# Performance work log

Measured on AMD Instinct MI355X. Metric: run time of the kernel, lower is better.

The kernel has to match this reference:

```python
import jax, jax.numpy as jnp
import numpy as np
from jax import lax

DIM = 128  # per-head dim used for scaling


def setup_inputs() -> dict:
    key = jax.random.key(0)
    ks = jax.random.split(key, 6)
    B, S, D = 16, 2048, DIM
    query = jax.random.normal(ks[0], (B, S, D), dtype=jnp.float32)
    k = jax.random.normal(ks[1], (B, S, D), dtype=jnp.float32)
    value = jax.random.normal(ks[2], (B, S, D), dtype=jnp.float32)
    mask = jax.random.randint(ks[3], (B, 1, S), 0, 2, dtype=jnp.int32)
    conv_w = jax.random.normal(ks[4], (B, 1, 3, 3), dtype=jnp.float32) * 0.1  # depthwise 3x3, OIHW
    conv_b = jax.random.normal(ks[5], (B,), dtype=jnp.float32) * 0.1
    return {"query": query, "key": k, "value": value, "mask": mask,
            "conv_w": conv_w, "conv_b": conv_b}


def reference(query, key, value, mask, conv_w, conv_b):
    B = query.shape[0]
    # score: (B, Sq, Sk)
    score = jnp.einsum('bqd,bkd->bqk', query, key) / jnp.float32(np.sqrt(DIM))
    # depthwise 3x3 conv over the score map; score treated as (C=B, H=Sq, W=Sk)
    conv = lax.conv_general_dilated(
        score[None],                      # (1, B, Sq, Sk)
        conv_w,                           # (B, 1, 3, 3)
        window_strides=(1, 1), padding='SAME',
        feature_group_count=B,
        dimension_numbers=('NCHW', 'OIHW', 'NCHW'))[0]
    conv = jax.nn.relu(conv + conv_b[:, None, None])
    conv_score = score + conv
    conv_score = jnp.where(mask == 0, jnp.float32(-1e9), conv_score)
    atten = jax.nn.softmax(conv_score, axis=-1)  # attn_drop=0.0 -> identity
    context = jnp.einsum('bqk,bkd->bqd', atten, value)
    return (context, atten)
```

## Files before the change

### kernel.cpp

```cpp
#include <hip/hip_runtime.h>
#include <stdint.h>

#define B_BATCH 16
#define SEQ     2048
#define DIMD    128
#define QT_OUT  14
#define SROWS   16
#define TILES_PB 147
#define SCALE   0.08838834764831845f
#define L2E     1.4426950408889634f

#define SC_STRIDE 4096
#define LDS_TOTAL (SROWS * SC_STRIDE)

typedef __attribute__((ext_vector_type(8))) short bf16x8;
typedef __attribute__((ext_vector_type(4))) float f32x4;

__device__ __forceinline__ unsigned short f2bf(float f) {
  union { float f; uint32_t u; } v; v.f = f;
  uint32_t u = v.u;
  return (unsigned short)((u + 0x7FFFu + ((u >> 16) & 1u)) >> 16);
}
__device__ __forceinline__ float bf2f(unsigned short h) {
  union { uint32_t u; float f; } v; v.u = ((uint32_t)h) << 16;
  return v.f;
}

__global__ __launch_bounds__(256) void cvt_bf16(const float* __restrict__ in,
                                                unsigned short* __restrict__ out) {
  const size_t i = (size_t)blockIdx.x * 256 + threadIdx.x;
  const float4 a = *(const float4*)(in + i * 8);
  const float4 b = *(const float4*)(in + i * 8 + 4);
  uint4 o;
  o.x = (uint32_t)f2bf(a.x) | ((uint32_t)f2bf(a.y) << 16);
  o.y = (uint32_t)f2bf(a.z) | ((uint32_t)f2bf(a.w) << 16);
  o.z = (uint32_t)f2bf(b.x) | ((uint32_t)f2bf(b.y) << 16);
  o.w = (uint32_t)f2bf(b.z) | ((uint32_t)f2bf(b.w) << 16);
  *(uint4*)(out + i * 8) = o;
}

__global__ __launch_bounds__(256) void transpose_v(const float* __restrict__ V,
                                                   unsigned short* __restrict__ Vt) {
  __shared__ float tl[64][65];
  const int b  = blockIdx.x >> 6;
  const int kt = (blockIdx.x & 63) >> 1;
  const int dt = blockIdx.x & 1;
  const int k0 = kt * 64, d0 = dt * 64;
  const int tid = threadIdx.x;
  const int r = tid >> 4, c4 = (tid & 15) * 4;
  const float* Vb = V + (size_t)b * SEQ * DIMD;
#pragma unroll
  for (int ii = 0; ii < 4; ++ii) {
    const int row = ii * 16 + r;
    float4 v = *(const float4*)(Vb + (size_t)(k0 + row) * DIMD + d0 + c4);
    tl[row][c4 + 0] = v.x; tl[row][c4 + 1] = v.y;
    tl[row][c4 + 2] = v.z; tl[row][c4 + 3] = v.w;
  }
  __syncthreads();
  unsigned short* VtB = Vt + (size_t)b * DIMD * SEQ;
#pragma unroll
  for (int ii = 0; ii < 4; ++ii) {
    const int drow = ii * 16 + r;
    ushort4 o;
    o.x = f2bf(tl[c4 + 0][drow]); o.y = f2bf(tl[c4 + 1][drow]);
    o.z = f2bf(tl[c4 + 2][drow]); o.w = f2bf(tl[c4 + 3][drow]);
    *(ushort4*)(VtB + (size_t)(d0 + drow) * SEQ + k0 + c4) = o;
  }
}

__global__ __launch_bounds__(512, 4) void fused_attn(
    const float* __restrict__ Q, const unsigned short* __restrict__ Kb,
    const unsigned short* __restrict__ Vt, const int* __restrict__ msk,
    const float* __restrict__ cw, const float* __restrict__ cbv,
    float* __restrict__ ctx, float* __restrict__ attn) {
  __shared__ __align__(16) char smem[LDS_TOTAL];

  const int bid = blockIdx.x;
  const int b  = bid / TILES_PB;
  const int t  = bid - b * TILES_PB;
  const int g0 = t * QT_OUT;
  const int tid = threadIdx.x;
  const int w = tid >> 6, lane = tid & 63, l15 = lane & 15, hi = lane >> 4;

  float w9[9];
#pragma unroll
  for (int i = 0; i < 9; ++i) w9[i] = cw[b * 9 + i];
  const float bias = cbv[b];

  uint32_t mb = 0;
  {
    const int* mp = msk + b * SEQ;
#pragma unroll
    for (int jb = 0; jb < 4; ++jb) {
      int4 a = *(const int4*)(mp + jb * 512 + lane * 8);
      int4 bq = *(const int4*)(mp + jb * 512 + lane * 8 + 4);
      mb |= (a.x  != 0 ? 1u : 0u) << (jb * 8 + 0);
      mb |= (a.y  != 0 ? 1u : 0u) << (jb * 8 + 1);
      mb |= (a.z  != 0 ? 1u : 0u) << (jb * 8 + 2);
      mb |= (a.w  != 0 ? 1u : 0u) << (jb * 8 + 3);
      mb |= (bq.x != 0 ? 1u : 0u) << (jb * 8 + 4);
      mb |= (bq.y != 0 ? 1u : 0u) << (jb * 8 + 5);
      mb |= (bq.z != 0 ? 1u : 0u) << (jb * 8 + 6);
      mb |= (bq.w != 0 ? 1u : 0u) << (jb * 8 + 7);
    }
  }

  bf16x8 aq[4];
  {
    int grow = g0 - 1 + l15;
    grow = grow < 0 ? 0 : (grow > SEQ - 1 ? SEQ - 1 : grow);
    const float* qp = Q + ((size_t)(b * SEQ + grow)) * DIMD + hi * 8;
#pragma unroll
    for (int ks = 0; ks < 4; ++ks) {
      float4 x = *(const float4*)(qp + ks * 32);
      float4 y = *(const float4*)(qp + ks * 32 + 4);
      bf16x8 f;
      f[0] = (short)f2bf(x.x); f[1] = (short)f2bf(x.y);
      f[2] = (short)f2bf(x.z); f[3] = (short)f2bf(x.w);
      f[4] = (short)f2bf(y.x); f[5] = (short)f2bf(y.y);
      f[6] = (short)f2bf(y.z); f[7] = (short)f2bf(y.w);
      aq[ks] = f;
    }
  }

  {
    const unsigned short* KbB = Kb + (size_t)b * SEQ * DIMD;
    const int k0w = w * 256;
#pragma unroll 2
    for (int kc = 0; kc < 16; ++kc) {
      const int k0 = k0w + kc * 16;
      const unsigned short* kp = KbB + (size_t)(k0 + l15) * DIMD + hi * 8;
      bf16x8 bk0 = *(const bf16x8*)(kp);
      bf16x8 bk1 = *(const bf16x8*)(kp + 32);
      bf16x8 bk2 = *(const bf16x8*)(kp + 64);
      bf16x8 bk3 = *(const bf16x8*)(kp + 96);
      f32x4 acc = {0.f, 0.f, 0.f, 0.f};
      acc = __builtin_amdgcn_mfma_f32_16x16x32_bf16(aq[0], bk0, acc, 0, 0, 0);
      acc = __builtin_amdgcn_mfma_f32_16x16x32_bf16(aq[1], bk1, acc, 0, 0, 0);
      acc = __builtin_amdgcn_mfma_f32_16x16x32_bf16(aq[2], bk2, acc, 0, 0, 0);
      acc = __builtin_amdgcn_mfma_f32_16x16x32_bf16(aq[3], bk3, acc, 0, 0, 0);
      const int colb = (k0 + l15) * 2;
#pragma unroll
      for (int r = 0; r < 4; ++r) {
        const int row = hi * 4 + r;
        *(unsigned short*)(smem + row * SC_STRIDE + (colb ^ ((row & 7) << 4))) =
            f2bf(acc[r] * SCALE);
      }
    }
  }
  __syncthreads();

  const int nrows = (SEQ - g0) < QT_OUT ? (SEQ - g0) : QT_OUT;
  float* attnB = attn + (size_t)b * SEQ * SEQ;

  for (int sp = 0; sp < 2; ++sp) {
    const int i = sp * 8 + w;
    const bool act = (i < nrows);
    float p[32];
    float inv = 0.f;
    if (act) {
      const int g = g0 + i;
      const bool vtop = (g > 0), vbot = (g + 1 < SEQ);
#pragma unroll
      for (int jb = 0; jb < 4; ++jb) {
        float m[3][8], Lv[3], Rv[3];
#pragma unroll
        for (int r = 0; r < 3; ++r) {
          const bool v = (r == 1) || ((r == 0) ? vtop : vbot);
          if (v) {
            const int row = i + r;
            const int rs = row * SC_STRIDE, sw = (row & 7) << 4;
            bf16x8 vv = *(const bf16x8*)(smem + rs + ((jb * 1024 + lane * 16) ^ sw));
#pragma unroll
            for (int c = 0; c < 8; ++c) m[r][c] = bf2f((unsigned short)vv[c]);
            float le = 0.f, re = 0.f;
            if (jb > 0)
              le = bf2f(*(const unsigned short*)(smem + rs + (((jb * 512 - 1) * 2) ^ sw)));
            if (jb < 3)
              re = bf2f(*(const unsigned short*)(smem + rs + (((jb * 512 + 512) * 2) ^ sw)));
            const float lsh = __shfl_up(m[r][7], 1);
            const float rsh = __shfl_down(m[r][0], 1);
            Lv[r] = (lane == 0)  ? le : lsh;
            Rv[r] = (lane == 63) ? re : rsh;
          } else {
#pragma unroll
            for (int c = 0; c < 8; ++c) m[r][c] = 0.f;
            Lv[r] = 0.f; Rv[r] = 0.f;
          }
        }
#pragma unroll
        for (int c = 0; c < 8; ++c) {
          float cv = 0.f;
#pragma unroll
          for (int r = 0; r < 3; ++r) {
            const float lft = (c == 0) ? Lv[r] : m[r][c - 1];
            const float rgt = (c == 7) ? Rv[r] : m[r][c + 1];
            cv += w9[r * 3 + 0] * lft + w9[r * 3 + 1] * m[r][c] + w9[r * 3 + 2] * rgt;
          }
          const float val = m[1][c] + fmaxf(cv + bias, 0.f);
          p[jb * 8 + c] = ((mb >> (jb * 8 + c)) & 1u) ? val : -1e9f;
        }
      }
      float mx = p[0];
#pragma unroll
      for (int k = 1; k < 32; ++k) mx = fmaxf(mx, p[k]);
#pragma unroll
      for (int o = 1; o < 64; o <<= 1) mx = fmaxf(mx, __shfl_xor(mx, o, 64));
      float Z = 0.f;
#pragma unroll
      for (int k = 0; k < 32; ++k) {
        p[k] = __builtin_amdgcn_exp2f((p[k] - mx) * L2E);
        Z += p[k];
      }
#pragma unroll
      for (int o = 1; o < 64; o <<= 1) Z += __shfl_xor(Z, o, 64);
      inv = 1.0f / Z;
      float* arow = attnB + (size_t)g * SEQ;
#pragma unroll
      for (int jb = 0; jb < 4; ++jb) {
        const int colb = jb * 512 + lane * 8;
        *(float4*)(arow + colb) = make_float4(p[jb * 8 + 0] * inv, p[jb * 8 + 1] * inv,
                                              p[jb * 8 + 2] * inv, p[jb * 8 + 3] * inv);
        *(float4*)(arow + colb + 4) = make_float4(p[jb * 8 + 4] * inv, p[jb * 8 + 5] * inv,
                                                  p[jb * 8 + 6] * inv, p[jb * 8 + 7] * inv);
      }
    }
    __syncthreads();
    if (act) {
      const int rs = i * SC_STRIDE, sw = (i & 7) << 4;
#pragma unroll
      for (int jb = 0; jb < 4; ++jb) {
        bf16x8 h;
#pragma unroll
        for (int c = 0; c < 8; ++c) h[c] = (short)f2bf(p[jb * 8 + c] * inv);
        *(bf16x8*)(smem + rs + ((jb * 1024 + lane * 16) ^ sw)) = h;
      }
    }
    __syncthreads();
  }

  {
    const unsigned short* vp =
        Vt + (size_t)b * DIMD * SEQ + (size_t)(16 * w + l15) * SEQ + hi * 8;
    const int arow = l15;
    const int abase = arow * SC_STRIDE;
    const int asw = (arow & 7) << 4;
    f32x4 acc0 = {0.f, 0.f, 0.f, 0.f}, acc1 = {0.f, 0.f, 0.f, 0.f};
#pragma unroll 2
    for (int kc = 0; kc < 32; ++kc) {
      const int k0 = kc * 64;
      bf16x8 a0 = *(const bf16x8*)(smem + abase + (((k0      ) * 2 + hi * 16) ^ asw));
      bf16x8 b0 = *(const bf16x8*)(vp + k0);
      acc0 = __builtin_amdgcn_mfma_f32_16x16x32_bf16(a0, b0, acc0, 0, 0, 0);
      bf16x8 a1 = *(const bf16x8*)(smem + abase + (((k0 + 32) * 2 + hi * 16) ^ asw));
      bf16x8 b1 = *(const bf16x8*)(vp + k0 + 32);
      acc1 = __builtin_amdgcn_mfma_f32_16x16x32_bf16(a1, b1, acc1, 0, 0, 0);
    }
    const int col = 16 * w + l15;
#pragma unroll
    for (int r = 0; r < 4; ++r) {
      const int row = hi * 4 + r;
      const int g = g0 + row;
      if (row < QT_OUT && g < SEQ)
        ctx[((size_t)(b * SEQ + g)) * DIMD + col] = acc0[r] + acc1[r];
    }
  }
}

extern "C" void kernel_launch(void* const* d_in, const int* in_sizes, int n_in,
                              void* d_out, int out_size, void* d_ws, size_t ws_size,
                              hipStream_t stream) {
  const float* Q  = (const float*)d_in[0];
  const float* K  = (const float*)d_in[1];
  const float* V  = (const float*)d_in[2];
  const int* msk  = (const int*)d_in[3];
  const float* cw = (const float*)d_in[4];
  const float* cb = (const float*)d_in[5];
  float* ctx  = (float*)d_out;
  float* attn = ctx + (size_t)B_BATCH * SEQ * DIMD;
  unsigned short* Kb = (unsigned short*)d_ws;
  unsigned short* Vt = Kb + (size_t)B_BATCH * SEQ * DIMD;

  cvt_bf16<<<2048, 256, 0, stream>>>(K, Kb);
  transpose_v<<<B_BATCH * 64, 256, 0, stream>>>(V, Vt);
  fused_attn<<<B_BATCH * TILES_PB, 512, 0, stream>>>(Q, Kb, Vt, msk, cw, cb, ctx, attn);
}
```

Baseline: 413.3 us.

## Defer attention-row stores to kernel end using nontemporal writes from LDS

New measurement: 366.9 us. 11.2% less time.

```diff
diff --git a/kernel.cpp b/kernel.cpp
--- a/kernel.cpp
+++ b/kernel.cpp
@@ -76,8 +76,8 @@
   __shared__ __align__(16) char smem[LDS_TOTAL];
 
   const int bid = blockIdx.x;
-  const int b  = bid / TILES_PB;
-  const int t  = bid - b * TILES_PB;
+  const int b  = bid & 15;
+  const int t  = bid >> 4;
   const int g0 = t * QT_OUT;
   const int tid = threadIdx.x;
   const int w = tid >> 6, lane = tid & 63, l15 = lane & 15, hi = lane >> 4;
@@ -126,7 +126,7 @@
   {
     const unsigned short* KbB = Kb + (size_t)b * SEQ * DIMD;
     const int k0w = w * 256;
-#pragma unroll 2
+#pragma unroll 4
     for (int kc = 0; kc < 16; ++kc) {
       const int k0 = k0w + kc * 16;
       const unsigned short* kp = KbB + (size_t)(k0 + l15) * DIMD + hi * 8;
@@ -151,7 +151,6 @@
   __syncthreads();
 
   const int nrows = (SEQ - g0) < QT_OUT ? (SEQ - g0) : QT_OUT;
-  float* attnB = attn + (size_t)b * SEQ * SEQ;
 
   for (int sp = 0; sp < 2; ++sp) {
     const int i = sp * 8 + w;
@@ -215,15 +214,6 @@
 #pragma unroll
       for (int o = 1; o < 64; o <<= 1) Z += __shfl_xor(Z, o, 64);
       inv = 1.0f / Z;
-      float* arow = attnB + (size_t)g * SEQ;
-#pragma unroll
-      for (int jb = 0; jb < 4; ++jb) {
-        const int colb = jb * 512 + lane * 8;
-        *(float4*)(arow + colb) = make_float4(p[jb * 8 + 0] * inv, p[jb * 8 + 1] * inv,
-                                              p[jb * 8 + 2] * inv, p[jb * 8 + 3] * inv);
-        *(float4*)(arow + colb + 4) = make_float4(p[jb * 8 + 4] * inv, p[jb * 8 + 5] * inv,
-                                                  p[jb * 8 + 6] * inv, p[jb * 8 + 7] * inv);
-      }
     }
     __syncthreads();
     if (act) {
@@ -242,11 +232,10 @@
   {
     const unsigned short* vp =
         Vt + (size_t)b * DIMD * SEQ + (size_t)(16 * w + l15) * SEQ + hi * 8;
-    const int arow = l15;
-    const int abase = arow * SC_STRIDE;
-    const int asw = (arow & 7) << 4;
+    const int abase = l15 * SC_STRIDE;
+    const int asw = (l15 & 7) << 4;
     f32x4 acc0 = {0.f, 0.f, 0.f, 0.f}, acc1 = {0.f, 0.f, 0.f, 0.f};
-#pragma unroll 2
+#pragma unroll 4
     for (int kc = 0; kc < 32; ++kc) {
       const int k0 = kc * 64;
       bf16x8 a0 = *(const bf16x8*)(smem + abase + (((k0      ) * 2 + hi * 16) ^ asw));
@@ -262,7 +251,31 @@
       const int row = hi * 4 + r;
       const int g = g0 + row;
       if (row < QT_OUT && g < SEQ)
-        ctx[((size_t)(b * SEQ + g)) * DIMD + col] = acc0[r] + acc1[r];
+        __builtin_nontemporal_store(acc0[r] + acc1[r],
+                                    &ctx[((size_t)(b * SEQ + g)) * DIMD + col]);
+    }
+  }
+
+  {
+    float* attnB = attn + (size_t)b * SEQ * SEQ;
+#pragma unroll
+    for (int sp = 0; sp < 2; ++sp) {
+      const int i = sp * 8 + w;
+      if (i < nrows) {
+        const int g = g0 + i;
+        float* arow = attnB + (size_t)g * SEQ;
+        const int rs = i * SC_STRIDE, sw = (i & 7) << 4;
+#pragma unroll
+        for (int jb = 0; jb < 8; ++jb) {
+          uint2 hv = *(const uint2*)(smem + rs + ((jb * 512 + lane * 8) ^ sw));
+          f32x4 o;
+          o[0] = bf2f((unsigned short)(hv.x & 0xffffu));
+          o[1] = bf2f((unsigned short)(hv.x >> 16));
+          o[2] = bf2f((unsigned short)(hv.y & 0xffffu));
+          o[3] = bf2f((unsigned short)(hv.y >> 16));
+          __builtin_nontemporal_store(o, (f32x4*)(arow + jb * 256 + lane * 4));
+        }
+      }
     }
   }
 }
```

## Split fused attention into separate QK GEMM, conv-softmax, and PV GEMM kernels

Applied to the files above, without the earlier changes.

New measurement: 425.5 us. +3.0%, slower.

```diff
diff --git a/kernel.cpp b/kernel.cpp
--- a/kernel.cpp
+++ b/kernel.cpp
@@ -4,14 +4,8 @@
 #define B_BATCH 16
 #define SEQ     2048
 #define DIMD    128
-#define QT_OUT  14
-#define SROWS   16
-#define TILES_PB 147
 #define SCALE   0.08838834764831845f
 #define L2E     1.4426950408889634f
-
-#define SC_STRIDE 4096
-#define LDS_TOTAL (SROWS * SC_STRIDE)
 
 typedef __attribute__((ext_vector_type(8))) short bf16x8;
 typedef __attribute__((ext_vector_type(4))) float f32x4;
@@ -68,19 +62,68 @@
   }
 }
 
-__global__ __launch_bounds__(512, 4) void fused_attn(
-    const float* __restrict__ Q, const unsigned short* __restrict__ Kb,
-    const unsigned short* __restrict__ Vt, const int* __restrict__ msk,
+__global__ __launch_bounds__(512, 2) void qk_gemm(
+    const unsigned short* __restrict__ Qb, const unsigned short* __restrict__ Kb,
+    unsigned short* __restrict__ S) {
+  __shared__ __align__(16) char sm[128 * 256];
+  const int bid = blockIdx.x;
+  const int b = bid & 15, t = bid >> 4, tr = t & 15, tc = t >> 4;
+  const int tid = threadIdx.x;
+  const int w = tid >> 6, lane = tid & 63, l15 = lane & 15, hi = lane >> 4;
+  const int wr = w >> 2, wc = w & 3;
+
+  const unsigned short* Qp =
+      Qb + ((size_t)(b * SEQ) + tr * 128 + wr * 64) * DIMD;
+  const unsigned short* Kp =
+      Kb + ((size_t)(b * SEQ) + tc * 128 + wc * 32) * DIMD;
+
+  f32x4 acc[4][2] = {};
+#pragma unroll
+  for (int ks = 0; ks < 4; ++ks) {
+    bf16x8 aq[4], bk[2];
+#pragma unroll
+    for (int fr = 0; fr < 4; ++fr)
+      aq[fr] = *(const bf16x8*)(Qp + (size_t)(fr * 16 + l15) * DIMD + ks * 32 + hi * 8);
+#pragma unroll
+    for (int fc = 0; fc < 2; ++fc)
+      bk[fc] = *(const bf16x8*)(Kp + (size_t)(fc * 16 + l15) * DIMD + ks * 32 + hi * 8);
+#pragma unroll
+    for (int fr = 0; fr < 4; ++fr)
+#pragma unroll
+      for (int fc = 0; fc < 2; ++fc)
+        acc[fr][fc] = __builtin_amdgcn_mfma_f32_16x16x32_bf16(aq[fr], bk[fc], acc[fr][fc], 0, 0, 0);
+  }
+#pragma unroll
+  for (int fr = 0; fr < 4; ++fr)
+#pragma unroll
+    for (int fc = 0; fc < 2; ++fc)
+#pragma unroll
+      for (int r = 0; r < 4; ++r) {
+        const int row = wr * 64 + fr * 16 + hi * 4 + r;
+        const int colb = (wc * 32 + fc * 16 + l15) * 2;
+        *(unsigned short*)(sm + row * 256 + (colb ^ ((row & 7) << 4))) =
+            f2bf(acc[fr][fc][r] * SCALE);
+      }
+  __syncthreads();
+  unsigned short* Sp = S + ((size_t)(b * SEQ) + tr * 128) * SEQ + tc * 128;
+  const int rr = tid >> 4, cc = tid & 15;
+#pragma unroll
+  for (int p = 0; p < 4; ++p) {
+    const int row = p * 32 + rr;
+    bf16x8 v = *(const bf16x8*)(sm + row * 256 + ((cc * 16) ^ ((row & 7) << 4)));
+    *(bf16x8*)(Sp + (size_t)row * SEQ + cc * 8) = v;
+  }
+}
+
+__global__ __launch_bounds__(512, 1) void conv_softmax(
+    const unsigned short* __restrict__ S, const int* __restrict__ msk,
     const float* __restrict__ cw, const float* __restrict__ cbv,
-    float* __restrict__ ctx, float* __restrict__ attn) {
-  __shared__ __align__(16) char smem[LDS_TOTAL];
-
+    float* __restrict__ attn) {
   const int bid = blockIdx.x;
-  const int b  = bid / TILES_PB;
-  const int t  = bid - b * TILES_PB;
-  const int g0 = t * QT_OUT;
-  const int tid = threadIdx.x;
-  const int w = tid >> 6, lane = tid & 63, l15 = lane & 15, hi = lane >> 4;
+  const int b = bid & 15, rblk = bid >> 4;
+  const int tid = threadIdx.x;
+  const int w = tid >> 6, lane = tid & 63;
+  const int g = rblk * 8 + w;
 
   float w9[9];
 #pragma unroll
@@ -105,166 +148,112 @@
     }
   }
 
-  bf16x8 aq[4];
-  {
-    int grow = g0 - 1 + l15;
-    grow = grow < 0 ? 0 : (grow > SEQ - 1 ? SEQ - 1 : grow);
-    const float* qp = Q + ((size_t)(b * SEQ + grow)) * DIMD + hi * 8;
-#pragma unroll
-    for (int ks = 0; ks < 4; ++ks) {
-      float4 x = *(const float4*)(qp + ks * 32);
-      float4 y = *(const float4*)(qp + ks * 32 + 4);
-      bf16x8 f;
-      f[0] = (short)f2bf(x.x); f[1] = (short)f2bf(x.y);
-      f[2] = (short)f2bf(x.z); f[3] = (short)f2bf(x.w);
-      f[4] = (short)f2bf(y.x); f[5] = (short)f2bf(y.y);
-      f[6] = (short)f2bf(y.z); f[7] = (short)f2bf(y.w);
-      aq[ks] = f;
-    }
-  }
-
-  {
-    const unsigned short* KbB = Kb + (size_t)b * SEQ * DIMD;
-    const int k0w = w * 256;
-#pragma unroll 2
-    for (int kc = 0; kc < 16; ++kc) {
-      const int k0 = k0w + kc * 16;
-      const unsigned short* kp = KbB + (size_t)(k0 + l15) * DIMD + hi * 8;
-      bf16x8 bk0 = *(const bf16x8*)(kp);
-      bf16x8 bk1 = *(const bf16x8*)(kp + 32);
-      bf16x8 bk2 = *(const bf16x8*)(kp + 64);
-      bf16x8 bk3 = *(const bf16x8*)(kp + 96);
-      f32x4 acc = {0.f, 0.f, 0.f, 0.f};
-      acc = __builtin_amdgcn_mfma_f32_16x16x32_bf16(aq[0], bk0, acc, 0, 0, 0);
-      acc = __builtin_amdgcn_mfma_f32_16x16x32_bf16(aq[1], bk1, acc, 0, 0, 0);
-      acc = __builtin_amdgcn_mfma_f32_16x16x32_bf16(aq[2], bk2, acc, 0, 0, 0);
-      acc = __builtin_amdgcn_mfma_f32_16x16x32_bf16(aq[3], bk3, acc, 0, 0, 0);
-      const int colb = (k0 + l15) * 2;
-#pragma unroll
-      for (int r = 0; r < 4; ++r) {
-        const int row = hi * 4 + r;
-        *(unsigned short*)(smem + row * SC_STRIDE + (colb ^ ((row & 7) << 4))) =
-            f2bf(acc[r] * SCALE);
+  const unsigned short* Sb = S + (size_t)b * SEQ * SEQ;
+  const bool vtop = (g > 0), vbot = (g + 1 < SEQ);
+  float p[32];
+#pragma unroll
+  for (int jb = 0; jb < 4; ++jb) {
+    float m[3][8], Lv[3], Rv[3];
+#pragma unroll
+    for (int r = 0; r < 3; ++r) {
+      const bool v = (r == 1) || ((r == 0) ? vtop : vbot);
+      if (v) {
+        const unsigned short* srow = Sb + (size_t)(g - 1 + r) * SEQ;
+        bf16x8 vv = *(const bf16x8*)(srow + jb * 512 + lane * 8);
+#pragma unroll
+        for (int c = 0; c < 8; ++c) m[r][c] = bf2f((unsigned short)vv[c]);
+        float le = 0.f, re = 0.f;
+        if (jb > 0) le = bf2f(srow[jb * 512 - 1]);
+        if (jb < 3) re = bf2f(srow[jb * 512 + 512]);
+        const float lsh = __shfl_up(m[r][7], 1);
+        const float rsh = __shfl_down(m[r][0], 1);
+        Lv[r] = (lane == 0)  ? le : lsh;
+        Rv[r] = (lane == 63) ? re : rsh;
+      } else {
+#pragma unroll
+        for (int c = 0; c < 8; ++c) m[r][c] = 0.f;
+        Lv[r] = 0.f; Rv[r] = 0.f;
       }
     }
-  }
-  __syncthreads();
-
-  const int nrows = (SEQ - g0) < QT_OUT ? (SEQ - g0) : QT_OUT;
-  float* attnB = attn + (size_t)b * SEQ * SEQ;
-
-  for (int sp = 0; sp < 2; ++sp) {
-    const int i = sp * 8 + w;
-    const bool act = (i < nrows);
-    float p[32];
-    float inv = 0.f;
-    if (act) {
-      const int g = g0 + i;
-      const bool vtop = (g > 0), vbot = (g + 1 < SEQ);
-#pragma unroll
-      for (int jb = 0; jb < 4; ++jb) {
-        float m[3][8], Lv[3], Rv[3];
-#pragma unroll
-        for (int r = 0; r < 3; ++r) {
-          const bool v = (r == 1) || ((r == 0) ? vtop : vbot);
-          if (v) {
-            const int row = i + r;
-            const int rs = row * SC_STRIDE, sw = (row & 7) << 4;
-            bf16x8 vv = *(const bf16x8*)(smem + rs + ((jb * 1024 + lane * 16) ^ sw));
-#pragma unroll
-            for (int c = 0; c < 8; ++c) m[r][c] = bf2f((unsigned short)vv[c]);
-            float le = 0.f, re = 0.f;
-            if (jb > 0)
-              le = bf2f(*(const unsigned short*)(smem + rs + (((jb * 512 - 1) * 2) ^ sw)));
-            if (jb < 3)
-              re = bf2f(*(const unsigned short*)(smem + rs + (((jb * 512 + 512) * 2) ^ sw)));
-            const float lsh = __shfl_up(m[r][7], 1);
-            const float rsh = __shfl_down(m[r][0], 1);
-            Lv[r] = (lane == 0)  ? le : lsh;
-            Rv[r] = (lane == 63) ? re : rsh;
-          } else {
-#pragma unroll
-            for (int c = 0; c < 8; ++c) m[r][c] = 0.f;
-            Lv[r] = 0.f; Rv[r] = 0.f;
-          }
-        }
-#pragma unroll
-        for (int c = 0; c < 8; ++c) {
-          float cv = 0.f;
-#pragma unroll
-          for (int r = 0; r < 3; ++r) {
-            const float lft = (c == 0) ? Lv[r] : m[r][c - 1];
-            const float rgt = (c == 7) ? Rv[r] : m[r][c + 1];
-            cv += w9[r * 3 + 0] * lft + w9[r * 3 + 1] * m[r][c] + w9[r * 3 + 2] * rgt;
-          }
-          const float val = m[1][c] + fmaxf(cv + bias, 0.f);
-          p[jb * 8 + c] = ((mb >> (jb * 8 + c)) & 1u) ? val : -1e9f;
-        }
+#pragma unroll
+    for (int c = 0; c < 8; ++c) {
+      float cv = 0.f;
+#pragma unroll
+      for (int r = 0; r < 3; ++r) {
+        const float lft = (c == 0) ? Lv[r] : m[r][c - 1];
+        const float rgt = (c == 7) ? Rv[r] : m[r][c + 1];
+        cv += w9[r * 3 + 0] * lft + w9[r * 3 + 1] * m[r][c] + w9[r * 3 + 2] * rgt;
       }
-      float mx = p[0];
-#pragma unroll
-      for (int k = 1; k < 32; ++k) mx = fmaxf(mx, p[k]);
-#pragma unroll
-      for (int o = 1; o < 64; o <<= 1) mx = fmaxf(mx, __shfl_xor(mx, o, 64));
-      float Z = 0.f;
-#pragma unroll
-      for (int k = 0; k < 32; ++k) {
-        p[k] = __builtin_amdgcn_exp2f((p[k] - mx) * L2E);
-        Z += p[k];
-      }
-#pragma unroll
-      for (int o = 1; o < 64; o <<= 1) Z += __shfl_xor(Z, o, 64);
-      inv = 1.0f / Z;
-      float* arow = attnB + (size_t)g * SEQ;
-#pragma unroll
-      for (int jb = 0; jb < 4; ++jb) {
-        const int colb = jb * 512 + lane * 8;
-        *(float4*)(arow + colb) = make_float4(p[jb * 8 + 0] * inv, p[jb * 8 + 1] * inv,
-                                              p[jb * 8 + 2] * inv, p[jb * 8 + 3] * inv);
-        *(float4*)(arow + colb + 4) = make_float4(p[jb * 8 + 4] * inv, p[jb * 8 + 5] * inv,
-                                                  p[jb * 8 + 6] * inv, p[jb * 8 + 7] * inv);
-      }
-    }
-    __syncthreads();
-    if (act) {
-      const int rs = i * SC_STRIDE, sw = (i & 7) << 4;
-#pragma unroll
-      for (int jb = 0; jb < 4; ++jb) {
-        bf16x8 h;
-#pragma unroll
-        for (int c = 0; c < 8; ++c) h[c] = (short)f2bf(p[jb * 8 + c] * inv);
-        *(bf16x8*)(smem + rs + ((jb * 1024 + lane * 16) ^ sw)) = h;
-      }
-    }
-    __syncthreads();
-  }
-
-  {
-    const unsigned short* vp =
-        Vt + (size_t)b * DIMD * SEQ + (size_t)(16 * w + l15) * SEQ + hi * 8;
-    const int arow = l15;
-    const int abase = arow * SC_STRIDE;
-    const int asw = (arow & 7) << 4;
-    f32x4 acc0 = {0.f, 0.f, 0.f, 0.f}, acc1 = {0.f, 0.f, 0.f, 0.f};
-#pragma unroll 2
-    for (int kc = 0; kc < 32; ++kc) {
-      const int k0 = kc * 64;
-      bf16x8 a0 = *(const bf16x8*)(smem + abase + (((k0      ) * 2 + hi * 16) ^ asw));
-      bf16x8 b0 = *(const bf16x8*)(vp + k0);
-      acc0 = __builtin_amdgcn_mfma_f32_16x16x32_bf16(a0, b0, acc0, 0, 0, 0);
-      bf16x8 a1 = *(const bf16x8*)(smem + abase + (((k0 + 32) * 2 + hi * 16) ^ asw));
-      bf16x8 b1 = *(const bf16x8*)(vp + k0 + 32);
-      acc1 = __builtin_amdgcn_mfma_f32_16x16x32_bf16(a1, b1, acc1, 0, 0, 0);
-    }
-    const int col = 16 * w + l15;
+      const float val = m[1][c] + fmaxf(cv + bias, 0.f);
+      p[jb * 8 + c] = ((mb >> (jb * 8 + c)) & 1u) ? val : -1e9f;
+    }
+  }
+  float mx = p[0];
+#pragma unroll
+  for (int k = 1; k < 32; ++k) mx = fmaxf(mx, p[k]);
+#pragma unroll
+  for (int o = 1; o < 64; o <<= 1) mx = fmaxf(mx, __shfl_xor(mx, o, 64));
+  float Z = 0.f;
+#pragma unroll
+  for (int k = 0; k < 32; ++k) {
+    p[k] = __builtin_amdgcn_exp2f((p[k] - mx) * L2E);
+    Z += p[k];
+  }
+#pragma unroll
+  for (int o = 1; o < 64; o <<= 1) Z += __shfl_xor(Z, o, 64);
+  const float inv = 1.0f / Z;
+
+  float* arow = attn + (size_t)b * SEQ * SEQ + (size_t)g * SEQ;
+#pragma unroll
+  for (int jb = 0; jb < 4; ++jb) {
+    f32x4 o0, o1;
+    o0[0] = p[jb * 8 + 0] * inv; o0[1] = p[jb * 8 + 1] * inv;
+    o0[2] = p[jb * 8 + 2] * inv; o0[3] = p[jb * 8 + 3] * inv;
+    o1[0] = p[jb * 8 + 4] * inv; o1[1] = p[jb * 8 + 5] * inv;
+    o1[2] = p[jb * 8 + 6] * inv; o1[3] = p[jb * 8 + 7] * inv;
+    __builtin_nontemporal_store(o0, (f32x4*)(arow + jb * 512 + lane * 8));
+    __builtin_nontemporal_store(o1, (f32x4*)(arow + jb * 512 + lane * 8 + 4));
+  }
+}
+
+__global__ __launch_bounds__(512, 2) void pv_gemm(
+    const float* __restrict__ attn, const unsigned short* __restrict__ Vt,
+    float* __restrict__ ctx) {
+  const int bid = blockIdx.x;
+  const int b = bid & 15, rt = bid >> 4;
+  const int tid = threadIdx.x;
+  const int w = tid >> 6, lane = tid & 63, l15 = lane & 15, hi = lane >> 4;
+  const int wr = w >> 1, wc = w & 1;
+
+  const float* Ap =
+      attn + ((size_t)b * SEQ + rt * 64 + wr * 16 + l15) * SEQ + hi * 8;
+  const unsigned short* Vp = Vt + ((size_t)b * DIMD + wc * 64) * SEQ;
+
+  f32x4 acc[4] = {};
+#pragma unroll 4
+  for (int kk = 0; kk < 64; ++kk) {
+    const int k0 = kk * 32;
+    float4 x = *(const float4*)(Ap + k0);
+    float4 y = *(const float4*)(Ap + k0 + 4);
+    bf16x8 a;
+    a[0] = (short)f2bf(x.x); a[1] = (short)f2bf(x.y);
+    a[2] = (short)f2bf(x.z); a[3] = (short)f2bf(x.w);
+    a[4] = (short)f2bf(y.x); a[5] = (short)f2bf(y.y);
+    a[6] = (short)f2bf(y.z); a[7] = (short)f2bf(y.w);
+#pragma unroll
+    for (int fc = 0; fc < 4; ++fc) {
+      bf16x8 bv = *(const bf16x8*)(Vp + (size_t)(fc * 16 + l15) * SEQ + k0 + hi * 8);
+      acc[fc] = __builtin_amdgcn_mfma_f32_16x16x32_bf16(a, bv, acc[fc], 0, 0, 0);
+    }
+  }
+#pragma unroll
+  for (int fc = 0; fc < 4; ++fc)
 #pragma unroll
     for (int r = 0; r < 4; ++r) {
-      const int row = hi * 4 + r;
-      const int g = g0 + row;
-      if (row < QT_OUT && g < SEQ)
-        ctx[((size_t)(b * SEQ + g)) * DIMD + col] = acc0[r] + acc1[r];
-    }
-  }
+      const int row = rt * 64 + wr * 16 + hi * 4 + r;
+      const int col = wc * 64 + fc * 16 + l15;
+      ctx[((size_t)b * SEQ + row) * DIMD + col] = acc[fc][r];
+    }
 }
 
 extern "C" void kernel_launch(void* const* d_in, const int* in_sizes, int n_in,
@@ -278,10 +267,17 @@
   const float* cb = (const float*)d_in[5];
   float* ctx  = (float*)d_out;
   float* attn = ctx + (size_t)B_BATCH * SEQ * DIMD;
-  unsigned short* Kb = (unsigned short*)d_ws;
-  unsigned short* Vt = Kb + (size_t)B_BATCH * SEQ * DIMD;
-
+
+  const size_t nQK = (size_t)B_BATCH * SEQ * DIMD;
+  unsigned short* Qb = (unsigned short*)d_ws;
+  unsigned short* Kb = Qb + nQK;
+  unsigned short* Vt = Kb + nQK;
+  unsigned short* S  = Vt + nQK;
+
+  cvt_bf16<<<2048, 256, 0, stream>>>(Q, Qb);
   cvt_bf16<<<2048, 256, 0, stream>>>(K, Kb);
   transpose_v<<<B_BATCH * 64, 256, 0, stream>>>(V, Vt);
-  fused_attn<<<B_BATCH * TILES_PB, 512, 0, stream>>>(Q, Kb, Vt, msk, cw, cb, ctx, attn);
-}
+  qk_gemm<<<4096, 512, 0, stream>>>(Qb, Kb, S);
+  conv_softmax<<<4096, 512, 0, stream>>>(S, msk, cw, cb, attn);
+  pv_gemm<<<512, 512, 0, stream>>>(attn, Vt, ctx);
+}
```
